# Performance work log

Measured on AMD Instinct MI355X. Metric: run time of the kernel, lower is better.

The kernel has to match this reference:

```python
import jax, jax.numpy as jnp
import numpy as np

# LIF constants from __init__ defaults and forward body
TAU = 20.0        # membrane time constant
TH = 1.0          # base threshold
TAU_ADAPT = 100.0 # adaptation time constant
BETA_ADAPT = 1.5  # adaptation strength
V_RESET = -0.5    # reset potential
K = 10.0          # surrogate sigmoid slope


def setup_inputs() -> dict:
    key = jax.random.key(0)
    I = jax.random.normal(key, (16384, 2048), dtype=jnp.float32)
    return {"I": I}


def reference(I):
    # I: (B, L). Sequential LIF recurrence over L via lax.scan.
    B, L = I.shape
    dtype = I.dtype

    def step(carry, I_t):
        v, a, s_num = carry  # each (B,)
        th_eff = TH + BETA_ADAPT * a
        v = v - v / TAU + I_t  # v += dv
        s_soft = jax.nn.sigmoid(K * (v - th_eff))
        s_hard = (v >= th_eff).astype(dtype)
        # straight-through: forward value = s_hard, grad flows via s_soft
        s = jax.lax.stop_gradient(s_hard - s_soft) + s_soft
        s_num = s_num + s
        s_det = jax.lax.stop_gradient(s)  # reset is non-differentiable (detached)
        v = v * (1.0 - s_det) + V_RESET * s_det
        a = a - a / TAU_ADAPT + s
        return (v, a, s_num), (s, s_num)

    zeros = jnp.zeros((B,), dtype)
    _, (spikes_t, series_t) = jax.lax.scan(step, (zeros, zeros, zeros), I.T)
    # scan outputs are (L, B); transpose back to (B, L)
    return spikes_t.T, series_t.T
```

## Files before the change

### kernel.cpp

```cpp
#include <hip/hip_runtime.h>


#define LIF_L  2048
#define TILE   64
#define NTILES (LIF_L / TILE)
#define STRIDE 65

__device__ __forceinline__ void barrier_lds_only() {
    asm volatile("s_waitcnt lgkmcnt(0)\n\ts_barrier" ::: "memory");
}

__device__ __forceinline__ float div20(float v) {
    const float rh = 0.05f;
    float q0 = __fmul_rn(v, rh);
    float r  = __fmaf_rn(-20.0f, q0, v);
    return __fmaf_rn(r, rh, q0);
}

__device__ __forceinline__ float div100(float a) {
    const float rh = 0.01f;
    float q0 = __fmul_rn(a, rh);
    float r  = __fmaf_rn(-100.0f, q0, a);
    return __fmaf_rn(r, rh, q0);
}

__device__ __forceinline__ float lif_step(float It, float& v, float& a) {
    float th = __fadd_rn(1.0f, __fmul_rn(1.5f, a));
    float vn = __fadd_rn(__fsub_rn(v, div20(v)), It);
    float ap  = __fsub_rn(a, div100(a));
    float ap1 = __fadd_rn(ap, 1.0f);
    bool fire = (vn >= th);
    v = fire ? -0.5f : vn;
    a = fire ? ap1 : ap;
    return fire ? 1.0f : 0.0f;
}

__global__ __launch_bounds__(128, 1) void lif_fwd(const float* __restrict__ I,
                                                  float* __restrict__ spikes,
                                                  float* __restrict__ series) {
    __shared__ float sp_tile[2][64 * STRIDE];
    __shared__ float se_tile[64 * STRIDE];

    const int tid  = threadIdx.x;
    const int wave = tid >> 6;
    const int lane = tid & 63;
    const int row0 = blockIdx.x * 64;

    const float4* __restrict__ I4 =
        reinterpret_cast<const float4*>(I + (size_t)(row0 + lane) * LIF_L);
    float v = 0.0f, a = 0.0f;
    float4 bufA[16], bufB[16];

    float carry = 0.0f;

    if (wave == 0) {
        #pragma unroll
        for (int i = 0; i < 16; ++i) bufA[i] = I4[i];
        #pragma unroll
        for (int i = 0; i < 16; ++i) bufB[i] = I4[16 + i];
    }

    auto compute_tile = [&](const float4* buf, float* sp) {
        #pragma unroll
        for (int c = 0; c < 16; ++c) {
            float4 in = buf[c];
            float s0 = lif_step(in.x, v, a);
            float s1 = lif_step(in.y, v, a);
            float s2 = lif_step(in.z, v, a);
            float s3 = lif_step(in.w, v, a);
            int b = lane * STRIDE + c * 4;
            sp[b + 0] = s0; sp[b + 1] = s1;
            sp[b + 2] = s2; sp[b + 3] = s3;
        }
    };

    auto helper_tile = [&](int tkt, const float* sp) {
        const int rb = lane * STRIDE;
        #pragma unroll
        for (int c = 0; c < 16; ++c) {
            float4 sv = make_float4(sp[rb + c*4], sp[rb + c*4 + 1],
                                    sp[rb + c*4 + 2], sp[rb + c*4 + 3]);
            float4 nv;
            carry = __fadd_rn(carry, sv.x); nv.x = carry;
            carry = __fadd_rn(carry, sv.y); nv.y = carry;
            carry = __fadd_rn(carry, sv.z); nv.z = carry;
            carry = __fadd_rn(carry, sv.w); nv.w = carry;
            se_tile[rb + c*4 + 0] = nv.x; se_tile[rb + c*4 + 1] = nv.y;
            se_tile[rb + c*4 + 2] = nv.z; se_tile[rb + c*4 + 3] = nv.w;
        }
        const size_t colbase = (size_t)tkt * TILE;
        #pragma unroll
        for (int i = 0; i < 16; ++i) {
            int idx = i * 64 + lane;
            int row = idx >> 4;
            int c4  = (idx & 15) * 4;
            int lb  = row * STRIDE + c4;
            float4 vs = make_float4(sp[lb], sp[lb + 1], sp[lb + 2], sp[lb + 3]);
            float4 ve = make_float4(se_tile[lb], se_tile[lb + 1],
                                    se_tile[lb + 2], se_tile[lb + 3]);
            size_t g = (size_t)(row0 + row) * LIF_L + colbase + c4;
            *reinterpret_cast<float4*>(spikes + g) = vs;
            *reinterpret_cast<float4*>(series + g) = ve;
        }
    };

    for (int kt = 0; kt < NTILES; kt += 2) {
        if (wave == 0) {
            compute_tile(bufA, sp_tile[0]);
            if (kt + 2 < NTILES) {
                #pragma unroll
                for (int i = 0; i < 16; ++i) bufA[i] = I4[(kt + 2) * 16 + i];
            }
        } else if (kt > 0) {
            helper_tile(kt - 1, sp_tile[1]);
        }
        barrier_lds_only();
        if (wave == 0) {
            compute_tile(bufB, sp_tile[1]);
            if (kt + 3 < NTILES) {
                #pragma unroll
                for (int i = 0; i < 16; ++i) bufB[i] = I4[(kt + 3) * 16 + i];
            }
        } else {
            helper_tile(kt, sp_tile[0]);
        }
        barrier_lds_only();
    }
    if (wave == 1) helper_tile(NTILES - 1, sp_tile[1]);
}

extern "C" void kernel_launch(void* const* d_in, const int* in_sizes, int n_in,
                              void* d_out, int out_size, void* d_ws, size_t ws_size,
                              hipStream_t stream) {
    const float* I = (const float*)d_in[0];
    const int B = in_sizes[0] / LIF_L;
    float* spikes = (float*)d_out;
    float* series = (float*)d_out + (size_t)B * LIF_L;

    const int threads = 128;
    const int blocks = B / 64;
    lif_fwd<<<blocks, threads, 0, stream>>>(I, spikes, series);
}
```

Baseline: 392.9 us.

## Skew LIF recurrence to shorten dependency chain and swizzle LDS tiles

Restructures the LIF step so the next input is added to the membrane potential inside the current step, and the threshold is precomputed from the updated adaptation. After a spike the potential becomes a precomputed constant plus the next input instead of passing through the reset select, which shortens the serial critical path per timestep. Separately, the padded LDS layout with stride 65 is replaced by an XOR-swizzled 64-wide layout, so spike and series tiles can use float4 LDS reads and writes instead of scalar ones. The skewed carry needs extra cross-tile plumbing to pass the next tile's first input, which adds complexity and some risk around boundaries.

```diff
diff --git a/kernel.cpp b/kernel.cpp
--- a/kernel.cpp
+++ b/kernel.cpp
@@ -4,42 +4,42 @@
 #define LIF_L  2048
 #define TILE   64
 #define NTILES (LIF_L / TILE)
-#define STRIDE 65
+
+constexpr float kR20 = -0.5f / 20.0f;
+constexpr float kC0  = -0.5f - kR20;
 
 __device__ __forceinline__ void barrier_lds_only() {
     asm volatile("s_waitcnt lgkmcnt(0)\n\ts_barrier" ::: "memory");
 }
 
-__device__ __forceinline__ float div20(float v) {
-    const float rh = 0.05f;
-    float q0 = __fmul_rn(v, rh);
-    float r  = __fmaf_rn(-20.0f, q0, v);
-    return __fmaf_rn(r, rh, q0);
+__device__ __forceinline__ float lif_step(float Inext, float& vn, float& a, float& th) {
+    bool fire = (vn >= th);
+    float s = fire ? 1.0f : 0.0f;
+    float q0 = __fmul_rn(vn, 0.05f);
+    float r  = __fmaf_rn(-20.0f, q0, vn);
+    float d  = __fmaf_rn(r, 0.05f, q0);
+    float ns = __fadd_rn(__fsub_rn(vn, d), Inext);
+    float ss = __fadd_rn(kC0, Inext);
+    vn = fire ? ss : ns;
+    float qa = __fmul_rn(a, 0.01f);
+    float ra = __fmaf_rn(-100.0f, qa, a);
+    float da = __fmaf_rn(ra, 0.01f, qa);
+    float ap  = __fsub_rn(a, da);
+    float ap1 = __fadd_rn(ap, 1.0f);
+    a = fire ? ap1 : ap;
+    th = __fadd_rn(1.0f, __fmul_rn(1.5f, a));
+    return s;
 }
 
-__device__ __forceinline__ float div100(float a) {
-    const float rh = 0.01f;
-    float q0 = __fmul_rn(a, rh);
-    float r  = __fmaf_rn(-100.0f, q0, a);
-    return __fmaf_rn(r, rh, q0);
-}
-
-__device__ __forceinline__ float lif_step(float It, float& v, float& a) {
-    float th = __fadd_rn(1.0f, __fmul_rn(1.5f, a));
-    float vn = __fadd_rn(__fsub_rn(v, div20(v)), It);
-    float ap  = __fsub_rn(a, div100(a));
-    float ap1 = __fadd_rn(ap, 1.0f);
-    bool fire = (vn >= th);
-    v = fire ? -0.5f : vn;
-    a = fire ? ap1 : ap;
-    return fire ? 1.0f : 0.0f;
+__device__ __forceinline__ int sw_idx(int row, int g) {
+    return row * 64 + (((g) ^ (row & 15)) << 2);
 }
 
 __global__ __launch_bounds__(128, 1) void lif_fwd(const float* __restrict__ I,
                                                   float* __restrict__ spikes,
                                                   float* __restrict__ series) {
-    __shared__ float sp_tile[2][64 * STRIDE];
-    __shared__ float se_tile[64 * STRIDE];
+    __shared__ float sp_tile[2][64 * 64];
+    __shared__ float se_tile[64 * 64];
 
     const int tid  = threadIdx.x;
     const int wave = tid >> 6;
@@ -48,9 +48,9 @@
 
     const float4* __restrict__ I4 =
         reinterpret_cast<const float4*>(I + (size_t)(row0 + lane) * LIF_L);
-    float v = 0.0f, a = 0.0f;
+
+    float vn = 0.0f, a = 0.0f, th = 1.0f;
     float4 bufA[16], bufB[16];
-
     float carry = 0.0f;
 
     if (wave == 0) {
@@ -60,53 +60,51 @@
         for (int i = 0; i < 16; ++i) bufB[i] = I4[16 + i];
     }
 
-    auto compute_tile = [&](const float4* buf, float* sp) {
+    auto compute_tile = [&](const float4* buf, float nx0, float* sp) {
         #pragma unroll
         for (int c = 0; c < 16; ++c) {
             float4 in = buf[c];
-            float s0 = lif_step(in.x, v, a);
-            float s1 = lif_step(in.y, v, a);
-            float s2 = lif_step(in.z, v, a);
-            float s3 = lif_step(in.w, v, a);
-            int b = lane * STRIDE + c * 4;
-            sp[b + 0] = s0; sp[b + 1] = s1;
-            sp[b + 2] = s2; sp[b + 3] = s3;
+            float nxt = (c < 15) ? buf[c + 1].x : nx0;
+            float4 os;
+            os.x = lif_step(in.y, vn, a, th);
+            os.y = lif_step(in.z, vn, a, th);
+            os.z = lif_step(in.w, vn, a, th);
+            os.w = lif_step(nxt,  vn, a, th);
+            *reinterpret_cast<float4*>(&sp[sw_idx(lane, c)]) = os;
         }
     };
 
     auto helper_tile = [&](int tkt, const float* sp) {
-        const int rb = lane * STRIDE;
         #pragma unroll
         for (int c = 0; c < 16; ++c) {
-            float4 sv = make_float4(sp[rb + c*4], sp[rb + c*4 + 1],
-                                    sp[rb + c*4 + 2], sp[rb + c*4 + 3]);
+            int ix = sw_idx(lane, c);
+            float4 sv = *reinterpret_cast<const float4*>(&sp[ix]);
             float4 nv;
             carry = __fadd_rn(carry, sv.x); nv.x = carry;
             carry = __fadd_rn(carry, sv.y); nv.y = carry;
             carry = __fadd_rn(carry, sv.z); nv.z = carry;
             carry = __fadd_rn(carry, sv.w); nv.w = carry;
-            se_tile[rb + c*4 + 0] = nv.x; se_tile[rb + c*4 + 1] = nv.y;
-            se_tile[rb + c*4 + 2] = nv.z; se_tile[rb + c*4 + 3] = nv.w;
+            *reinterpret_cast<float4*>(&se_tile[ix]) = nv;
         }
         const size_t colbase = (size_t)tkt * TILE;
         #pragma unroll
         for (int i = 0; i < 16; ++i) {
-            int idx = i * 64 + lane;
-            int row = idx >> 4;
-            int c4  = (idx & 15) * 4;
-            int lb  = row * STRIDE + c4;
-            float4 vs = make_float4(sp[lb], sp[lb + 1], sp[lb + 2], sp[lb + 3]);
-            float4 ve = make_float4(se_tile[lb], se_tile[lb + 1],
-                                    se_tile[lb + 2], se_tile[lb + 3]);
-            size_t g = (size_t)(row0 + row) * LIF_L + colbase + c4;
-            *reinterpret_cast<float4*>(spikes + g) = vs;
-            *reinterpret_cast<float4*>(series + g) = ve;
+            int row = i * 4 + (lane >> 4);
+            int g   = lane & 15;
+            int ix  = sw_idx(row, g);
+            float4 vs = *reinterpret_cast<const float4*>(&sp[ix]);
+            float4 ve = *reinterpret_cast<const float4*>(&se_tile[ix]);
+            size_t gaddr = (size_t)(row0 + row) * LIF_L + colbase + (size_t)g * 4;
+            *reinterpret_cast<float4*>(spikes + gaddr) = vs;
+            *reinterpret_cast<float4*>(series + gaddr) = ve;
         }
     };
 
+    if (wave == 0) vn = bufA[0].x;
+
     for (int kt = 0; kt < NTILES; kt += 2) {
         if (wave == 0) {
-            compute_tile(bufA, sp_tile[0]);
+            compute_tile(bufA, bufB[0].x, sp_tile[0]);
             if (kt + 2 < NTILES) {
                 #pragma unroll
                 for (int i = 0; i < 16; ++i) bufA[i] = I4[(kt + 2) * 16 + i];
@@ -116,7 +114,8 @@
         }
         barrier_lds_only();
         if (wave == 0) {
-            compute_tile(bufB, sp_tile[1]);
+            float nx0 = (kt + 2 < NTILES) ? bufA[0].x : 0.0f;
+            compute_tile(bufB, nx0, sp_tile[1]);
             if (kt + 3 < NTILES) {
                 #pragma unroll
                 for (int i = 0; i < 16; ++i) bufB[i] = I4[(kt + 3) * 16 + i];
```

After: 382.4 us. 2.7% less time.
